# Kernel optimization log

Measured on AMD Instinct MI355X. Metric: run time of the kernel, lower is better.

Reference implementation:

```python
import jax, jax.numpy as jnp
import numpy as np

B, T, IN, H, OUT = 64, 512, 256, 1024, 1


def _uniform(key, shape, k):
    return jax.random.uniform(key, shape, jnp.float32, -k, k)


def setup_inputs() -> dict:
    key = jax.random.key(0)
    ks = jax.random.split(key, 12)
    k = 1.0 / np.sqrt(H)
    return {
        "x": jax.random.normal(ks[0], (B, T, IN), jnp.float32),
        "W_ih0": _uniform(ks[1], (3 * H, IN), k),
        "W_hh0": _uniform(ks[2], (3 * H, H), k),
        "b_ih0": _uniform(ks[3], (3 * H,), k),
        "b_hh0": _uniform(ks[4], (3 * H,), k),
        "W_ih1": _uniform(ks[5], (3 * H, H), k),
        "W_hh1": _uniform(ks[6], (3 * H, H), k),
        "b_ih1": _uniform(ks[7], (3 * H,), k),
        "b_hh1": _uniform(ks[8], (3 * H,), k),
        "W_fc": _uniform(ks[9], (OUT, H), 1.0 / np.sqrt(H)),
        "b_fc": _uniform(ks[10], (OUT,), 1.0 / np.sqrt(H)),
    }


def _gru_layer(x, W_ih, W_hh, b_ih, b_hh):
    # x: [B, T, D_in] -> outputs [B, T, H], final hidden [B, H]
    # Precompute input projections for all timesteps (one big GEMM).
    xg = jnp.einsum('btd,gd->btg', x, W_ih) + b_ih  # [B, T, 3H]
    xg = jnp.swapaxes(xg, 0, 1)  # [T, B, 3H]

    def step(h, xg_t):
        hg = h @ W_hh.T + b_hh  # [B, 3H]
        xr, xz, xn = jnp.split(xg_t, 3, axis=-1)
        hr, hz, hn = jnp.split(hg, 3, axis=-1)
        r = jax.nn.sigmoid(xr + hr)
        z = jax.nn.sigmoid(xz + hz)
        n = jnp.tanh(xn + r * hn)
        h_new = (1.0 - z) * n + z * h
        return h_new, h_new

    h0 = jnp.zeros((x.shape[0], W_hh.shape[1]), x.dtype)
    h_final, ys = jax.lax.scan(step, h0, xg)
    return jnp.swapaxes(ys, 0, 1), h_final


def reference(x, W_ih0, W_hh0, b_ih0, b_hh0, W_ih1, W_hh1, b_ih1, b_hh1, W_fc, b_fc):
    # Inference mode: dropout (between GRU layers and before fc) is identity.
    y0, _ = _gru_layer(x, W_ih0, W_hh0, b_ih0, b_hh0)
    _, h_last = _gru_layer(y0, W_ih1, W_hh1, b_ih1, b_hh1)
    return h_last @ W_fc.T + b_fc  # [B, OUT]
```

## Files before the change

### kernel.cpp

```cpp
#include <hip/hip_runtime.h>
#include <hip/hip_bf16.h>
#include <stdint.h>


constexpr int TSEQ = 512;
constexpr int NB   = 64;
constexpr int HD   = 1024;
constexpr int IND  = 256;
constexpr int NWG  = 256;
constexpr int FS   = 16;
constexpr int PL   = NB * HD;

typedef float f32x4  __attribute__((ext_vector_type(4)));
typedef short short8 __attribute__((ext_vector_type(8)));

__device__ __forceinline__ float bf2f(unsigned u) {
    return __builtin_bit_cast(float, u << 16);
}
__device__ __forceinline__ unsigned short f2bf(float f) {
    unsigned u = __builtin_bit_cast(unsigned, f);
    u += 0x7fffu + ((u >> 16) & 1u);
    return (unsigned short)(u >> 16);
}
__device__ __forceinline__ float sigm(float x) { return 1.0f / (1.0f + __expf(-x)); }
__device__ __forceinline__ float tanh_fast(float x) { return 1.0f - 2.0f / (1.0f + __expf(2.0f * x)); }

__device__ __forceinline__ void cstore16(unsigned short* p, unsigned short v) {
    __hip_atomic_store(p, v, __ATOMIC_RELAXED, __HIP_MEMORY_SCOPE_AGENT);
}
__device__ __forceinline__ unsigned short cload16(const unsigned short* p) {
    return __hip_atomic_load(p, __ATOMIC_RELAXED, __HIP_MEMORY_SCOPE_AGENT);
}

#define MFMA(a, b, c) __builtin_amdgcn_mfma_f32_16x16x32_bf16((a), (b), (c), 0, 0, 0)

#define LDA16(dst, base, imm) \
    asm volatile("global_load_dwordx4 %0, %1, off offset:%2 sc0 sc1" \
                 : "=v"(dst) : "v"(base), "i"(imm))
#define LDX16(dst, base, imm) \
    asm volatile("global_load_dwordx4 %0, %1, off offset:%2" \
                 : "=v"(dst) : "v"(base), "i"(imm))
#define VWAIT(n) do { asm volatile("s_waitcnt vmcnt(" #n ")" ::: "memory"); \
                      __builtin_amdgcn_sched_barrier(0); } while (0)

__global__ void convert_w(const float* __restrict__ src, unsigned short* __restrict__ dst, int n) {
    int i = blockIdx.x * blockDim.x + threadIdx.x;
    int stride = gridDim.x * blockDim.x;
    for (; i < n; i += stride) dst[i] = f2bf(src[i]);
}

__global__ __launch_bounds__(512, 2) void gru_main(
    const float* __restrict__ x,
    const unsigned short* __restrict__ wih0,
    const unsigned short* __restrict__ whh0,
    const unsigned short* __restrict__ wih1,
    const unsigned short* __restrict__ whh1,
    const float* __restrict__ bih0, const float* __restrict__ bhh0,
    const float* __restrict__ bih1, const float* __restrict__ bhh1,
    const float* __restrict__ wfc,  const float* __restrict__ bfc,
    unsigned short* __restrict__ h0hi, unsigned short* __restrict__ h0lo,
    unsigned short* __restrict__ h1hi, unsigned short* __restrict__ h1lo,
    int* __restrict__ lvl0, int* __restrict__ lvl1, int* __restrict__ rel,
    float* __restrict__ out)
{
    const int wg    = blockIdx.x;
    const int layer = wg >> 7;
    const int cc    = wg & 127;
    const int jb8   = cc << 3;
    const int tid   = threadIdx.x;
    const int wid   = tid >> 6;
    const int kh    = wid >> 2;
    const int mw    = wid & 3;
    const int lane  = tid & 63;
    const int l15   = lane & 15;
    const int c8    = l15 & 7;
    const int kg8   = (lane >> 4) << 3;
    const int arow  = (mw << 4) + l15;
    const int kb    = kh << 9;
    const int ckb   = kh << 4;
    const int kbx   = kh << 7;

    const unsigned short* Whh = layer ? whh1 : whh0;
    const unsigned short* Wih = layer ? wih1 : wih0;
    const float* bih = layer ? bih1 : bih0;
    const float* bhh = layer ? bhh1 : bhh0;
    unsigned short* hhi = layer ? h1hi : h0hi;
    unsigned short* hlo = layer ? h1lo : h0lo;

    const int jg = jb8 + c8;

    const float bias_r  = bih[jg]        + bhh[jg];
    const float bias_z  = bih[HD + jg]   + bhh[HD + jg];
    const float bias_nx = bih[2*HD + jg];
    const float bias_nh = bhh[2*HD + jg];

    __shared__ unsigned short wlds[192 * 256];
    __shared__ float part[16 * 4 * 64];
    __shared__ float red[256];

    if (layer == 1) {
        #pragma unroll
        for (int i = 0; i < 12; ++i) {
            int f = tid + i * 512;
            int s   = f >> 10;
            int rem = f & 1023;
            int ck  = rem >> 5;
            int hi  = (rem >> 3) & 3;
            int c   = rem & 7;
            const unsigned short* src = (s < 3 ? Whh : Wih)
                + (size_t)((s % 3) * HD + jb8 + c) * HD + ck * 32 + hi * 8;
            *(short8*)(wlds + (s * 32 + ck) * 256 + hi * 64 + c * 8) =
                *(const short8*)src;
        }
    } else {
        #pragma unroll
        for (int i = 0; i < 6; ++i) {
            int f = tid + i * 512;
            int s   = f >> 10;
            int rem = f & 1023;
            int ck  = rem >> 5;
            int hi  = (rem >> 3) & 3;
            int c   = rem & 7;
            const unsigned short* src = Whh
                + (size_t)(s * HD + jb8 + c) * HD + ck * 32 + hi * 8;
            *(short8*)(wlds + (s * 32 + ck) * 256 + hi * 64 + c * 8) =
                *(const short8*)src;
        }
        for (int i = 0; i < 2; ++i) {
            int f = tid + i * 512;
            if (f < 768) {
                int s   = f >> 8;
                int rem = f & 255;
                int ck  = rem >> 5;
                int hi  = (rem >> 3) & 3;
                int c   = rem & 7;
                const unsigned short* src = Wih
                    + (size_t)(s * HD + jb8 + c) * IND + ck * 32 + hi * 8;
                *(short8*)(wlds + (96 + s * 8 + ck) * 256 + hi * 64 + c * 8) =
                    *(const short8*)src;
            }
        }
    }
    __syncthreads();

    const int lws = (lane >> 4) * 64 + c8 * 8;
#define LW(blk) (*(const short8*)(wlds + (blk) * 256 + lws))

    float hold[4] = {0.f, 0.f, 0.f, 0.f};

    for (int iter = 0; iter <= TSEQ; ++iter) {
        const bool active = layer ? (iter >= 1) : (iter < TSEQ);
        if (active) {
            const int t     = layer ? (iter - 1) : iter;
            const int rs    = (t + 1) & 1;
            const int wslot = t & 1;
            const unsigned short* hrhi = hhi + rs * PL;
            const unsigned short* hrlo = hlo + rs * PL;
            const unsigned short* bAh = hrhi + (size_t)arow * HD + kb + kg8;
            const unsigned short* bAl = hrlo + (size_t)arow * HD + kb + kg8;

            f32x4 ar  = {0.f, 0.f, 0.f, 0.f};
            f32x4 az  = {0.f, 0.f, 0.f, 0.f};
            f32x4 ahn = {0.f, 0.f, 0.f, 0.f};
            f32x4 axn = {0.f, 0.f, 0.f, 0.f};

            if (layer == 0) {
                const float* px = x + ((size_t)arow * TSEQ + t) * IND + kbx + kg8;
                short8 Ah[8], Al[8], Wa[3], Wb[3];
#define L0A(c) do { LDA16(Ah[(c)%8], bAh, (c)*64); LDA16(Al[(c)%8], bAl, (c)*64); } while (0)
#define L0X(c) do { LDX16(Ah[(c)%8], px, ((c)-16)*128); LDX16(Al[(c)%8], px, ((c)-16)*128+16); } while (0)
#define WR0(c, WB) do { WB[0] = LW(ckb + (c)); WB[1] = LW(32 + ckb + (c)); \
                        WB[2] = LW(64 + ckb + (c)); } while (0)
#define WX0(c, WB) do { int xck = (ckb >> 2) + (c) - 16; \
                        WB[0] = LW(96 + xck); WB[1] = LW(104 + xck); \
                        WB[2] = LW(112 + xck); } while (0)
#define MR0(c, WB) do { \
    ar  = MFMA(Ah[(c)%8], WB[0], ar);  ar  = MFMA(Al[(c)%8], WB[0], ar);  \
    az  = MFMA(Ah[(c)%8], WB[1], az);  az  = MFMA(Al[(c)%8], WB[1], az);  \
    ahn = MFMA(Ah[(c)%8], WB[2], ahn); ahn = MFMA(Al[(c)%8], WB[2], ahn); } while (0)
#define MX0(c, WB) do { \
    float4 xa = __builtin_bit_cast(float4, Ah[(c)%8]); \
    float4 xc = __builtin_bit_cast(float4, Al[(c)%8]); \
    short8 af; \
    af[0] = (short)f2bf(xa.x); af[1] = (short)f2bf(xa.y); \
    af[2] = (short)f2bf(xa.z); af[3] = (short)f2bf(xa.w); \
    af[4] = (short)f2bf(xc.x); af[5] = (short)f2bf(xc.y); \
    af[6] = (short)f2bf(xc.z); af[7] = (short)f2bf(xc.w); \
    ar  = MFMA(af, WB[0], ar); \
    az  = MFMA(af, WB[1], az); \
    axn = MFMA(af, WB[2], axn); } while (0)
                WR0(0, Wa);
                L0A(0); L0A(1); L0A(2); L0A(3); L0A(4); L0A(5); L0A(6);
                WR0(1,  Wb); L0A(7);  VWAIT(14); MR0(0,  Wa);
                WR0(2,  Wa); L0A(8);  VWAIT(14); MR0(1,  Wb);
                WR0(3,  Wb); L0A(9);  VWAIT(14); MR0(2,  Wa);
                WR0(4,  Wa); L0A(10); VWAIT(14); MR0(3,  Wb);
                WR0(5,  Wb); L0A(11); VWAIT(14); MR0(4,  Wa);
                WR0(6,  Wa); L0A(12); VWAIT(14); MR0(5,  Wb);
                WR0(7,  Wb); L0A(13); VWAIT(14); MR0(6,  Wa);
                WR0(8,  Wa); L0A(14); VWAIT(14); MR0(7,  Wb);
                WR0(9,  Wb); L0A(15); VWAIT(14); MR0(8,  Wa);
                WR0(10, Wa); L0X(16); VWAIT(14); MR0(9,  Wb);
                WR0(11, Wb); L0X(17); VWAIT(14); MR0(10, Wa);
                WR0(12, Wa); L0X(18); VWAIT(14); MR0(11, Wb);
                WR0(13, Wb); L0X(19); VWAIT(14); MR0(12, Wa);
                WR0(14, Wa);          VWAIT(12); MR0(13, Wb);
                WR0(15, Wb);          VWAIT(10); MR0(14, Wa);
                WX0(16, Wa);          VWAIT(8);  MR0(15, Wb);
                WX0(17, Wb);          VWAIT(6);  MX0(16, Wa);
                WX0(18, Wa);          VWAIT(4);  MX0(17, Wb);
                WX0(19, Wb);          VWAIT(2);  MX0(18, Wa);
                                      VWAIT(0);  MX0(19, Wb);
            } else {
                const unsigned short* bAy = h0hi + (size_t)wslot * PL
                                                 + (size_t)arow * HD + kb + kg8;
                short8 Ah[8], Al[8], Ay[8], Wa[6], Wb[6];
#define L1A(c) do { LDA16(Ah[(c)%8], bAh, (c)*64); LDA16(Al[(c)%8], bAl, (c)*64); \
                    LDA16(Ay[(c)%8], bAy, (c)*64); } while (0)
#define WR1(c, WB) do { WB[0] = LW(ckb + (c)); WB[1] = LW(32 + ckb + (c)); \
    WB[2] = LW(64 + ckb + (c)); WB[3] = LW(96 + ckb + (c)); \
    WB[4] = LW(128 + ckb + (c)); WB[5] = LW(160 + ckb + (c)); } while (0)
#define MF1(c, WB) do { \
    ar  = MFMA(Ah[(c)%8], WB[0], ar);  ar  = MFMA(Al[(c)%8], WB[0], ar);  \
    ar  = MFMA(Ay[(c)%8], WB[3], ar); \
    az  = MFMA(Ah[(c)%8], WB[1], az);  az  = MFMA(Al[(c)%8], WB[1], az);  \
    az  = MFMA(Ay[(c)%8], WB[4], az); \
    ahn = MFMA(Ah[(c)%8], WB[2], ahn); ahn = MFMA(Al[(c)%8], WB[2], ahn); \
    axn = MFMA(Ay[(c)%8], WB[5], axn); } while (0)
                WR1(0, Wa);
                L1A(0); L1A(1); L1A(2); L1A(3); L1A(4); L1A(5); L1A(6);
                WR1(1,  Wb); L1A(7);  VWAIT(21); MF1(0,  Wa);
                WR1(2,  Wa); L1A(8);  VWAIT(21); MF1(1,  Wb);
                WR1(3,  Wb); L1A(9);  VWAIT(21); MF1(2,  Wa);
                WR1(4,  Wa); L1A(10); VWAIT(21); MF1(3,  Wb);
                WR1(5,  Wb); L1A(11); VWAIT(21); MF1(4,  Wa);
                WR1(6,  Wa); L1A(12); VWAIT(21); MF1(5,  Wb);
                WR1(7,  Wb); L1A(13); VWAIT(21); MF1(6,  Wa);
                WR1(8,  Wa); L1A(14); VWAIT(21); MF1(7,  Wb);
                WR1(9,  Wb); L1A(15); VWAIT(21); MF1(8,  Wa);
                WR1(10, Wa);          VWAIT(18); MF1(9,  Wb);
                WR1(11, Wb);          VWAIT(15); MF1(10, Wa);
                WR1(12, Wa);          VWAIT(12); MF1(11, Wb);
                WR1(13, Wb);          VWAIT(9);  MF1(12, Wa);
                WR1(14, Wa);          VWAIT(6);  MF1(13, Wb);
                WR1(15, Wb);          VWAIT(3);  MF1(14, Wa);
                                      VWAIT(0);  MF1(15, Wb);
            }

            if (kh) {
                #pragma unroll
                for (int e = 0; e < 4; ++e) {
                    part[((0*4 + e) * 4 + mw) * 64 + lane] = ar[e];
                    part[((1*4 + e) * 4 + mw) * 64 + lane] = az[e];
                    part[((2*4 + e) * 4 + mw) * 64 + lane] = ahn[e];
                    part[((3*4 + e) * 4 + mw) * 64 + lane] = axn[e];
                }
            }
            __syncthreads();
            if (!kh) {
                unsigned short* hwhi = hhi + wslot * PL;
                unsigned short* hwlo = hlo + wslot * PL;
                #pragma unroll
                for (int e = 0; e < 4; ++e) {
                    const float arr = ar[e]  + part[((0*4 + e) * 4 + mw) * 64 + lane];
                    const float azz = az[e]  + part[((1*4 + e) * 4 + mw) * 64 + lane];
                    const float ahh = ahn[e] + part[((2*4 + e) * 4 + mw) * 64 + lane];
                    const float axx = axn[e] + part[((3*4 + e) * 4 + mw) * 64 + lane];
                    const int bat = (mw << 4) + ((lane >> 4) << 2) + e;
                    const size_t idx = (size_t)bat * HD + jg;
                    float r = sigm(arr + bias_r);
                    float z = sigm(azz + bias_z);
                    float n = tanh_fast(axx + bias_nx + r * (ahh + bias_nh));
                    float hnew = (1.0f - z) * n + z * hold[e];
                    hold[e] = hnew;
                    if (l15 < 8) {
                        unsigned short hi_ = f2bf(hnew);
                        cstore16(hwhi + idx, hi_);
                        cstore16(hwlo + idx, f2bf(hnew - bf2f((unsigned)hi_)));
                    }
                }
            }
        }

        asm volatile("s_waitcnt vmcnt(0)" ::: "memory");
        __syncthreads();
        if (tid == 0) {
            const int g = wg >> 3;
            int* l0p = lvl0 + ((size_t)iter * 32 + g) * FS;
            int old = __hip_atomic_fetch_add(l0p, 1, __ATOMIC_RELAXED,
                                             __HIP_MEMORY_SCOPE_AGENT);
            if (old == 7) {
                int old2 = __hip_atomic_fetch_add(lvl1 + (size_t)iter * FS, 1,
                                                  __ATOMIC_RELAXED,
                                                  __HIP_MEMORY_SCOPE_AGENT);
                if (old2 == 31) {
                    #pragma unroll
                    for (int k = 0; k < 32; ++k)
                        __hip_atomic_store(rel + ((size_t)iter * 32 + k) * FS, 1,
                                           __ATOMIC_RELAXED,
                                           __HIP_MEMORY_SCOPE_AGENT);
                }
            }
            int* rp = rel + ((size_t)iter * 32 + g) * FS;
            int spins = 0;
            while (__hip_atomic_load(rp, __ATOMIC_RELAXED,
                                     __HIP_MEMORY_SCOPE_AGENT) < 1) {
                __builtin_amdgcn_s_sleep(2);
                if (++spins > (1 << 20)) break;
            }
        }
        __syncthreads();
    }

    if (wg == 0) {
        const int fslot = (TSEQ - 1) & 1;
        const unsigned short* hf_hi = h1hi + (size_t)fslot * PL;
        const unsigned short* hf_lo = h1lo + (size_t)fslot * PL;
        if (tid < 256) {
            const int bat  = tid & 63;
            const int pidx = tid >> 6;
            const int k0   = pidx * (HD / 4);
            float s = 0.0f;
            for (int k = 0; k < HD / 4; ++k) {
                size_t idx = (size_t)bat * HD + k0 + k;
                s += (bf2f((unsigned)cload16(hf_hi + idx)) +
                      bf2f((unsigned)cload16(hf_lo + idx))) * wfc[k0 + k];
            }
            red[tid] = s;
        }
        __syncthreads();
        if (tid < 64)
            out[tid] = red[tid] + red[tid + 64] + red[tid + 128] + red[tid + 192] + bfc[0];
    }
}

extern "C" void kernel_launch(void* const* d_in, const int* in_sizes, int n_in,
                              void* d_out, int out_size, void* d_ws, size_t ws_size,
                              hipStream_t stream) {
    const float* x    = (const float*)d_in[0];
    const float* Wih0 = (const float*)d_in[1];
    const float* Whh0 = (const float*)d_in[2];
    const float* bih0 = (const float*)d_in[3];
    const float* bhh0 = (const float*)d_in[4];
    const float* Wih1 = (const float*)d_in[5];
    const float* Whh1 = (const float*)d_in[6];
    const float* bih1 = (const float*)d_in[7];
    const float* bhh1 = (const float*)d_in[8];
    const float* Wfc  = (const float*)d_in[9];
    const float* bfc  = (const float*)d_in[10];
    float* out = (float*)d_out;

    char* ws = (char*)d_ws;
    size_t off = 0;
    int* lvl0 = (int*)(ws + off); off += (size_t)(TSEQ + 1) * 32 * FS * 4;
    int* lvl1 = (int*)(ws + off); off += (size_t)(TSEQ + 1) * FS * 4;
    int* rel  = (int*)(ws + off); off += (size_t)(TSEQ + 1) * 32 * FS * 4;
    unsigned short* h0hi = (unsigned short*)(ws + off); off += (size_t)2 * PL * 2;
    unsigned short* h0lo = (unsigned short*)(ws + off); off += (size_t)2 * PL * 2;
    unsigned short* h1hi = (unsigned short*)(ws + off); off += (size_t)2 * PL * 2;
    unsigned short* h1lo = (unsigned short*)(ws + off); off += (size_t)2 * PL * 2;
    size_t zero_bytes = off;
    unsigned short* wih0b = (unsigned short*)(ws + off); off += (size_t)3 * HD * IND * 2;
    unsigned short* whh0b = (unsigned short*)(ws + off); off += (size_t)3 * HD * HD * 2;
    unsigned short* wih1b = (unsigned short*)(ws + off); off += (size_t)3 * HD * HD * 2;
    unsigned short* whh1b = (unsigned short*)(ws + off); off += (size_t)3 * HD * HD * 2;
    if (off > ws_size) return;

    hipMemsetAsync(d_ws, 0, zero_bytes, stream);
    hipMemsetAsync(d_out, 0, (size_t)out_size * sizeof(float), stream);

    convert_w<<<512, 256, 0, stream>>>(Wih0, wih0b, 3 * HD * IND);
    convert_w<<<512, 256, 0, stream>>>(Whh0, whh0b, 3 * HD * HD);
    convert_w<<<512, 256, 0, stream>>>(Wih1, wih1b, 3 * HD * HD);
    convert_w<<<512, 256, 0, stream>>>(Whh1, whh1b, 3 * HD * HD);

    gru_main<<<NWG, 512, 0, stream>>>(x, wih0b, whh0b, wih1b, whh1b,
                                      bih0, bhh0, bih1, bhh1, Wfc, bfc,
                                      h0hi, h0lo, h1hi, h1lo,
                                      lvl0, lvl1, rel, out);
}
```

Measured before the change: 7.094 ms.

## Split K reduction across four wave groups with 1024-thread blocks

Doubles the workgroup to 1024 threads so the per-step recurrent GEMV is split four ways along K instead of two. Each wave does half the MFMA chain and holds fewer prefetch registers, which shortens per-step latency on the serial critical path. The partial sums are reduced through LDS as vector writes from three quarters. The cost is more LDS reduction traffic, a larger barrier, and higher register pressure under the 1024-thread launch bound.

```diff
diff --git a/kernel.cpp b/kernel.cpp
--- a/kernel.cpp
+++ b/kernel.cpp
@@ -49,7 +49,7 @@
     for (; i < n; i += stride) dst[i] = f2bf(src[i]);
 }
 
-__global__ __launch_bounds__(512, 2) void gru_main(
+__global__ __launch_bounds__(1024, 4) void gru_main(
     const float* __restrict__ x,
     const unsigned short* __restrict__ wih0,
     const unsigned short* __restrict__ whh0,
@@ -69,16 +69,15 @@
     const int jb8   = cc << 3;
     const int tid   = threadIdx.x;
     const int wid   = tid >> 6;
-    const int kh    = wid >> 2;
+    const int kq    = wid >> 2;
     const int mw    = wid & 3;
     const int lane  = tid & 63;
     const int l15   = lane & 15;
     const int c8    = l15 & 7;
     const int kg8   = (lane >> 4) << 3;
     const int arow  = (mw << 4) + l15;
-    const int kb    = kh << 9;
-    const int ckb   = kh << 4;
-    const int kbx   = kh << 7;
+    const int kb    = kq << 8;
+    const int ckb   = kq << 3;
 
     const unsigned short* Whh = layer ? whh1 : whh0;
     const unsigned short* Wih = layer ? wih1 : wih0;
@@ -95,13 +94,13 @@
     const float bias_nh = bhh[2*HD + jg];
 
     __shared__ unsigned short wlds[192 * 256];
-    __shared__ float part[16 * 4 * 64];
+    __shared__ f32x4 partv[3 * 4 * 4 * 64];
     __shared__ float red[256];
 
     if (layer == 1) {
         #pragma unroll
-        for (int i = 0; i < 12; ++i) {
-            int f = tid + i * 512;
+        for (int i = 0; i < 6; ++i) {
+            int f = tid + i * 1024;
             int s   = f >> 10;
             int rem = f & 1023;
             int ck  = rem >> 5;
@@ -114,8 +113,8 @@
         }
     } else {
         #pragma unroll
-        for (int i = 0; i < 6; ++i) {
-            int f = tid + i * 512;
+        for (int i = 0; i < 3; ++i) {
+            int f = tid + i * 1024;
             int s   = f >> 10;
             int rem = f & 1023;
             int ck  = rem >> 5;
@@ -126,19 +125,16 @@
             *(short8*)(wlds + (s * 32 + ck) * 256 + hi * 64 + c * 8) =
                 *(const short8*)src;
         }
-        for (int i = 0; i < 2; ++i) {
-            int f = tid + i * 512;
-            if (f < 768) {
-                int s   = f >> 8;
-                int rem = f & 255;
-                int ck  = rem >> 5;
-                int hi  = (rem >> 3) & 3;
-                int c   = rem & 7;
-                const unsigned short* src = Wih
-                    + (size_t)(s * HD + jb8 + c) * IND + ck * 32 + hi * 8;
-                *(short8*)(wlds + (96 + s * 8 + ck) * 256 + hi * 64 + c * 8) =
-                    *(const short8*)src;
-            }
+        if (tid < 768) {
+            int s   = tid >> 8;
+            int rem = tid & 255;
+            int ck  = rem >> 5;
+            int hi  = (rem >> 3) & 3;
+            int c   = rem & 7;
+            const unsigned short* src = Wih
+                + (size_t)(s * HD + jb8 + c) * IND + ck * 32 + hi * 8;
+            *(short8*)(wlds + (96 + s * 8 + ck) * 256 + hi * 64 + c * 8) =
+                *(const short8*)src;
         }
     }
     __syncthreads();
@@ -165,22 +161,22 @@
             f32x4 axn = {0.f, 0.f, 0.f, 0.f};
 
             if (layer == 0) {
-                const float* px = x + ((size_t)arow * TSEQ + t) * IND + kbx + kg8;
-                short8 Ah[8], Al[8], Wa[3], Wb[3];
-#define L0A(c) do { LDA16(Ah[(c)%8], bAh, (c)*64); LDA16(Al[(c)%8], bAl, (c)*64); } while (0)
-#define L0X(c) do { LDX16(Ah[(c)%8], px, ((c)-16)*128); LDX16(Al[(c)%8], px, ((c)-16)*128+16); } while (0)
+                const float* px = x + ((size_t)arow * TSEQ + t) * IND + (kq << 6) + kg8;
+                short8 Ah[3], Al[3], Wa[3], Wb[3];
+#define L0A(c) do { LDA16(Ah[(c)%3], bAh, (c)*64); LDA16(Al[(c)%3], bAl, (c)*64); } while (0)
+#define L0X(c) do { LDX16(Ah[(c)%3], px, ((c)-8)*128); LDX16(Al[(c)%3], px, ((c)-8)*128+16); } while (0)
 #define WR0(c, WB) do { WB[0] = LW(ckb + (c)); WB[1] = LW(32 + ckb + (c)); \
                         WB[2] = LW(64 + ckb + (c)); } while (0)
-#define WX0(c, WB) do { int xck = (ckb >> 2) + (c) - 16; \
+#define WX0(c, WB) do { int xck = (kq << 1) + (c) - 8; \
                         WB[0] = LW(96 + xck); WB[1] = LW(104 + xck); \
                         WB[2] = LW(112 + xck); } while (0)
 #define MR0(c, WB) do { \
-    ar  = MFMA(Ah[(c)%8], WB[0], ar);  ar  = MFMA(Al[(c)%8], WB[0], ar);  \
-    az  = MFMA(Ah[(c)%8], WB[1], az);  az  = MFMA(Al[(c)%8], WB[1], az);  \
-    ahn = MFMA(Ah[(c)%8], WB[2], ahn); ahn = MFMA(Al[(c)%8], WB[2], ahn); } while (0)
+    ar  = MFMA(Ah[(c)%3], WB[0], ar);  ar  = MFMA(Al[(c)%3], WB[0], ar);  \
+    az  = MFMA(Ah[(c)%3], WB[1], az);  az  = MFMA(Al[(c)%3], WB[1], az);  \
+    ahn = MFMA(Ah[(c)%3], WB[2], ahn); ahn = MFMA(Al[(c)%3], WB[2], ahn); } while (0)
 #define MX0(c, WB) do { \
-    float4 xa = __builtin_bit_cast(float4, Ah[(c)%8]); \
-    float4 xc = __builtin_bit_cast(float4, Al[(c)%8]); \
+    float4 xa = __builtin_bit_cast(float4, Ah[(c)%3]); \
+    float4 xc = __builtin_bit_cast(float4, Al[(c)%3]); \
     short8 af; \
     af[0] = (short)f2bf(xa.x); af[1] = (short)f2bf(xa.y); \
     af[2] = (short)f2bf(xa.z); af[3] = (short)f2bf(xa.w); \
@@ -190,87 +186,71 @@
     az  = MFMA(af, WB[1], az); \
     axn = MFMA(af, WB[2], axn); } while (0)
                 WR0(0, Wa);
-                L0A(0); L0A(1); L0A(2); L0A(3); L0A(4); L0A(5); L0A(6);
-                WR0(1,  Wb); L0A(7);  VWAIT(14); MR0(0,  Wa);
-                WR0(2,  Wa); L0A(8);  VWAIT(14); MR0(1,  Wb);
-                WR0(3,  Wb); L0A(9);  VWAIT(14); MR0(2,  Wa);
-                WR0(4,  Wa); L0A(10); VWAIT(14); MR0(3,  Wb);
-                WR0(5,  Wb); L0A(11); VWAIT(14); MR0(4,  Wa);
-                WR0(6,  Wa); L0A(12); VWAIT(14); MR0(5,  Wb);
-                WR0(7,  Wb); L0A(13); VWAIT(14); MR0(6,  Wa);
-                WR0(8,  Wa); L0A(14); VWAIT(14); MR0(7,  Wb);
-                WR0(9,  Wb); L0A(15); VWAIT(14); MR0(8,  Wa);
-                WR0(10, Wa); L0X(16); VWAIT(14); MR0(9,  Wb);
-                WR0(11, Wb); L0X(17); VWAIT(14); MR0(10, Wa);
-                WR0(12, Wa); L0X(18); VWAIT(14); MR0(11, Wb);
-                WR0(13, Wb); L0X(19); VWAIT(14); MR0(12, Wa);
-                WR0(14, Wa);          VWAIT(12); MR0(13, Wb);
-                WR0(15, Wb);          VWAIT(10); MR0(14, Wa);
-                WX0(16, Wa);          VWAIT(8);  MR0(15, Wb);
-                WX0(17, Wb);          VWAIT(6);  MX0(16, Wa);
-                WX0(18, Wa);          VWAIT(4);  MX0(17, Wb);
-                WX0(19, Wb);          VWAIT(2);  MX0(18, Wa);
-                                      VWAIT(0);  MX0(19, Wb);
+                L0A(0); L0A(1);
+                WR0(1, Wb); L0A(2); VWAIT(4); MR0(0, Wa);
+                WR0(2, Wa); L0A(3); VWAIT(4); MR0(1, Wb);
+                WR0(3, Wb); L0A(4); VWAIT(4); MR0(2, Wa);
+                WR0(4, Wa); L0A(5); VWAIT(4); MR0(3, Wb);
+                WR0(5, Wb); L0A(6); VWAIT(4); MR0(4, Wa);
+                WR0(6, Wa); L0A(7); VWAIT(4); MR0(5, Wb);
+                WR0(7, Wb); L0X(8); VWAIT(4); MR0(6, Wa);
+                WX0(8, Wa); L0X(9); VWAIT(4); MR0(7, Wb);
+                WX0(9, Wb);         VWAIT(2); MX0(8, Wa);
+                                    VWAIT(0); MX0(9, Wb);
             } else {
                 const unsigned short* bAy = h0hi + (size_t)wslot * PL
                                                  + (size_t)arow * HD + kb + kg8;
-                short8 Ah[8], Al[8], Ay[8], Wa[6], Wb[6];
-#define L1A(c) do { LDA16(Ah[(c)%8], bAh, (c)*64); LDA16(Al[(c)%8], bAl, (c)*64); \
-                    LDA16(Ay[(c)%8], bAy, (c)*64); } while (0)
+                short8 Ah[3], Al[3], Ay[3], Wa[6], Wb[6];
+#define L1A(c) do { LDA16(Ah[(c)%3], bAh, (c)*64); LDA16(Al[(c)%3], bAl, (c)*64); \
+                    LDA16(Ay[(c)%3], bAy, (c)*64); } while (0)
 #define WR1(c, WB) do { WB[0] = LW(ckb + (c)); WB[1] = LW(32 + ckb + (c)); \
     WB[2] = LW(64 + ckb + (c)); WB[3] = LW(96 + ckb + (c)); \
     WB[4] = LW(128 + ckb + (c)); WB[5] = LW(160 + ckb + (c)); } while (0)
 #define MF1(c, WB) do { \
-    ar  = MFMA(Ah[(c)%8], WB[0], ar);  ar  = MFMA(Al[(c)%8], WB[0], ar);  \
-    ar  = MFMA(Ay[(c)%8], WB[3], ar); \
-    az  = MFMA(Ah[(c)%8], WB[1], az);  az  = MFMA(Al[(c)%8], WB[1], az);  \
-    az  = MFMA(Ay[(c)%8], WB[4], az); \
-    ahn = MFMA(Ah[(c)%8], WB[2], ahn); ahn = MFMA(Al[(c)%8], WB[2], ahn); \
-    axn = MFMA(Ay[(c)%8], WB[5], axn); } while (0)
+    ar  = MFMA(Ah[(c)%3], WB[0], ar);  ar  = MFMA(Al[(c)%3], WB[0], ar);  \
+    ar  = MFMA(Ay[(c)%3], WB[3], ar); \
+    az  = MFMA(Ah[(c)%3], WB[1], az);  az  = MFMA(Al[(c)%3], WB[1], az);  \
+    az  = MFMA(Ay[(c)%3], WB[4], az); \
+    ahn = MFMA(Ah[(c)%3], WB[2], ahn); ahn = MFMA(Al[(c)%3], WB[2], ahn); \
+    axn = MFMA(Ay[(c)%3], WB[5], axn); } while (0)
                 WR1(0, Wa);
-                L1A(0); L1A(1); L1A(2); L1A(3); L1A(4); L1A(5); L1A(6);
-                WR1(1,  Wb); L1A(7);  VWAIT(21); MF1(0,  Wa);
-                WR1(2,  Wa); L1A(8);  VWAIT(21); MF1(1,  Wb);
-                WR1(3,  Wb); L1A(9);  VWAIT(21); MF1(2,  Wa);
-                WR1(4,  Wa); L1A(10); VWAIT(21); MF1(3,  Wb);
-                WR1(5,  Wb); L1A(11); VWAIT(21); MF1(4,  Wa);
-                WR1(6,  Wa); L1A(12); VWAIT(21); MF1(5,  Wb);
-                WR1(7,  Wb); L1A(13); VWAIT(21); MF1(6,  Wa);
-                WR1(8,  Wa); L1A(14); VWAIT(21); MF1(7,  Wb);
-                WR1(9,  Wb); L1A(15); VWAIT(21); MF1(8,  Wa);
-                WR1(10, Wa);          VWAIT(18); MF1(9,  Wb);
-                WR1(11, Wb);          VWAIT(15); MF1(10, Wa);
-                WR1(12, Wa);          VWAIT(12); MF1(11, Wb);
-                WR1(13, Wb);          VWAIT(9);  MF1(12, Wa);
-                WR1(14, Wa);          VWAIT(6);  MF1(13, Wb);
-                WR1(15, Wb);          VWAIT(3);  MF1(14, Wa);
-                                      VWAIT(0);  MF1(15, Wb);
-            }
-
-            if (kh) {
+                L1A(0); L1A(1);
+                WR1(1, Wb); L1A(2); VWAIT(6); MF1(0, Wa);
+                WR1(2, Wa); L1A(3); VWAIT(6); MF1(1, Wb);
+                WR1(3, Wb); L1A(4); VWAIT(6); MF1(2, Wa);
+                WR1(4, Wa); L1A(5); VWAIT(6); MF1(3, Wb);
+                WR1(5, Wb); L1A(6); VWAIT(6); MF1(4, Wa);
+                WR1(6, Wa); L1A(7); VWAIT(6); MF1(5, Wb);
+                WR1(7, Wb);         VWAIT(3); MF1(6, Wa);
+                                    VWAIT(0); MF1(7, Wb);
+            }
+
+            if (kq) {
+                const int pb = (((kq - 1) * 4 + 0) * 4 + mw) * 64 + lane;
+                partv[pb]           = ar;
+                partv[pb + 1 * 256] = az;
+                partv[pb + 2 * 256] = ahn;
+                partv[pb + 3 * 256] = axn;
+            }
+            __syncthreads();
+            if (!kq) {
                 #pragma unroll
-                for (int e = 0; e < 4; ++e) {
-                    part[((0*4 + e) * 4 + mw) * 64 + lane] = ar[e];
-                    part[((1*4 + e) * 4 + mw) * 64 + lane] = az[e];
-                    part[((2*4 + e) * 4 + mw) * 64 + lane] = ahn[e];
-                    part[((3*4 + e) * 4 + mw) * 64 + lane] = axn[e];
+                for (int q = 0; q < 3; ++q) {
+                    const int pb = ((q * 4 + 0) * 4 + mw) * 64 + lane;
+                    ar  += partv[pb];
+                    az  += partv[pb + 1 * 256];
+                    ahn += partv[pb + 2 * 256];
+                    axn += partv[pb + 3 * 256];
                 }
-            }
-            __syncthreads();
-            if (!kh) {
                 unsigned short* hwhi = hhi + wslot * PL;
                 unsigned short* hwlo = hlo + wslot * PL;
                 #pragma unroll
                 for (int e = 0; e < 4; ++e) {
-                    const float arr = ar[e]  + part[((0*4 + e) * 4 + mw) * 64 + lane];
-                    const float azz = az[e]  + part[((1*4 + e) * 4 + mw) * 64 + lane];
-                    const float ahh = ahn[e] + part[((2*4 + e) * 4 + mw) * 64 + lane];
-                    const float axx = axn[e] + part[((3*4 + e) * 4 + mw) * 64 + lane];
                     const int bat = (mw << 4) + ((lane >> 4) << 2) + e;
                     const size_t idx = (size_t)bat * HD + jg;
-                    float r = sigm(arr + bias_r);
-                    float z = sigm(azz + bias_z);
-                    float n = tanh_fast(axx + bias_nx + r * (ahh + bias_nh));
+                    float r = sigm(ar[e] + bias_r);
+                    float z = sigm(az[e] + bias_z);
+                    float n = tanh_fast(axn[e] + bias_nx + r * (ahn[e] + bias_nh));
                     float hnew = (1.0f - z) * n + z * hold[e];
                     hold[e] = hnew;
                     if (l15 < 8) {
@@ -374,8 +354,8 @@
     convert_w<<<512, 256, 0, stream>>>(Wih1, wih1b, 3 * HD * HD);
     convert_w<<<512, 256, 0, stream>>>(Whh1, whh1b, 3 * HD * HD);
 
-    gru_main<<<NWG, 512, 0, stream>>>(x, wih0b, whh0b, wih1b, whh1b,
-                                      bih0, bhh0, bih1, bhh1, Wfc, bfc,
-                                      h0hi, h0lo, h1hi, h1lo,
-                                      lvl0, lvl1, rel, out);
-}
+    gru_main<<<NWG, 1024, 0, stream>>>(x, wih0b, whh0b, wih1b, whh1b,
+                                       bih0, bhh0, bih1, bhh1, Wfc, bfc,
+                                       h0hi, h0lo, h1hi, h1lo,
+                                       lvl0, lvl1, rel, out);
+}
```

New measurement: 8.158 ms. 15.0% more time.
